# Kernel tuning notes

Measured on AMD Instinct MI355X. Metric: run time of the kernel, lower is better.

Reference implementation:

```python
import jax, jax.numpy as jnp
import numpy as np

B, C, H, W = 8, 3, 64, 64
HORIZON = 32
WIDTH = 32
M1 = M2 = M3 = 8
N_LAYERS = 4
C_OUT = 3


def setup_inputs() -> dict:
    key = jax.random.key(0)
    ks = jax.random.split(key, 16)
    scale = 1.0 / (WIDTH * WIDTH)
    wshape = (N_LAYERS, 4, WIDTH, WIDTH, M1, M2, M3)
    return {
        "x_t": jax.random.normal(ks[0], (B, C, H, W), dtype=jnp.float32),
        "p_w": jax.random.normal(ks[1], (WIDTH, C + 3), dtype=jnp.float32) * 0.1,
        "p_b": jnp.zeros((WIDTH,), dtype=jnp.float32),
        "spec_wr": scale * jax.random.normal(ks[2], wshape, dtype=jnp.float32),
        "spec_wi": scale * jax.random.normal(ks[3], wshape, dtype=jnp.float32),
        "pw_w": jax.random.normal(ks[4], (N_LAYERS, WIDTH, WIDTH), dtype=jnp.float32) * 0.1,
        "pw_b": jnp.zeros((N_LAYERS, WIDTH), dtype=jnp.float32),
        "q1_w": jax.random.normal(ks[5], (2 * WIDTH, WIDTH), dtype=jnp.float32) * 0.1,
        "q1_b": jnp.zeros((2 * WIDTH,), dtype=jnp.float32),
        "q2_w": jax.random.normal(ks[6], (C_OUT, 2 * WIDTH), dtype=jnp.float32) * 0.1,
        "q2_b": jnp.zeros((C_OUT,), dtype=jnp.float32),
        "horizon": HORIZON,
    }


def _conv1x1(x, w, b):
    # x: [b, i, x, y, z], w: [o, i] -> [b, o, x, y, z]
    return jnp.einsum("oi,bixyz->boxyz", w, x) + b[None, :, None, None, None]


def _spectral_conv3d(x, wr, wi):
    # x: [b, i, H, W, T]; wr/wi: [4, i, o, m1, m2, m3]
    h, w_, t = x.shape[-3], x.shape[-2], x.shape[-1]
    xf = jnp.fft.rfftn(x, axes=(-3, -2, -1))  # [b, i, H, W, T//2+1]
    wc = (wr + 1j * wi).astype(xf.dtype)
    m1 = min(M1, xf.shape[-3]); m2 = min(M2, xf.shape[-2]); m3 = min(M3, xf.shape[-1])
    mul = lambda a, ww: jnp.einsum("bixyz,ioxyz->boxyz", a, ww)
    out = jnp.zeros((x.shape[0], wr.shape[2]) + xf.shape[2:], dtype=xf.dtype)
    out = out.at[:, :, :m1, :m2, :m3].set(mul(xf[:, :, :m1, :m2, :m3], wc[0, :, :, :m1, :m2, :m3]))
    out = out.at[:, :, -m1:, :m2, :m3].set(mul(xf[:, :, -m1:, :m2, :m3], wc[1, :, :, :m1, :m2, :m3]))
    out = out.at[:, :, :m1, -m2:, :m3].set(mul(xf[:, :, :m1, -m2:, :m3], wc[2, :, :, :m1, :m2, :m3]))
    out = out.at[:, :, -m1:, -m2:, :m3].set(mul(xf[:, :, -m1:, -m2:, :m3], wc[3, :, :, :m1, :m2, :m3]))
    return jnp.fft.irfftn(out, s=(h, w_, t), axes=(-3, -2, -1))


def _grid_3d(b, h, w, t, dtype):
    gy = jnp.broadcast_to(jnp.linspace(0.0, 1.0, h, dtype=dtype)[None, None, :, None, None], (b, 1, h, w, t))
    gx = jnp.broadcast_to(jnp.linspace(0.0, 1.0, w, dtype=dtype)[None, None, None, :, None], (b, 1, h, w, t))
    gt = jnp.broadcast_to(jnp.linspace(0.0, 1.0, t, dtype=dtype)[None, None, None, None, :], (b, 1, h, w, t))
    return jnp.concatenate([gy, gx, gt], axis=1)


def reference(x_t, p_w, p_b, spec_wr, spec_wi, pw_w, pw_b, q1_w, q1_b, q2_w, q2_b, horizon):
    b, c, h, w = x_t.shape
    x = jnp.broadcast_to(x_t[..., None], (b, c, h, w, horizon))  # repeat over time
    grid = _grid_3d(b, h, w, horizon, x_t.dtype)
    x = jnp.concatenate([x, grid], axis=1)  # [b, c+3, h, w, t]
    x = _conv1x1(x, p_w, p_b)
    for l in range(N_LAYERS):
        x = jax.nn.gelu(
            _spectral_conv3d(x, spec_wr[l], spec_wi[l]) + _conv1x1(x, pw_w[l], pw_b[l]),
            approximate=False,
        )
    x = _conv1x1(x, q1_w, q1_b)
    x = jax.nn.gelu(x, approximate=False)
    x = _conv1x1(x, q2_w, q2_b)
    # [b, c_out, h, w, t] -> [b, t, c_out, h, w]
    return jnp.transpose(x, (0, 4, 1, 2, 3))
```

## Files before the change

kernel.cpp:

```cpp
#include <hip/hip_runtime.h>
#include <math.h>


#define TWO_PI 6.2831853071795864769f

typedef short bf16x8 __attribute__((ext_vector_type(8)));
typedef float f32x4 __attribute__((ext_vector_type(4)));
typedef float v2f __attribute__((ext_vector_type(2)));

__device__ __forceinline__ f32x4 mfma16(bf16x8 a, bf16x8 b, f32x4 c) {
    return __builtin_amdgcn_mfma_f32_16x16x32_bf16(a, b, c, 0, 0, 0);
}

__device__ __forceinline__ void split8(float4 a, float4 b, bf16x8& h, bf16x8& l) {
    float f[8] = {a.x, a.y, a.z, a.w, b.x, b.y, b.z, b.w};
    #pragma unroll
    for (int i = 0; i < 8; ++i) {
        unsigned u = __float_as_uint(f[i]);
        h[i] = (short)(u >> 16);
        float hf = __uint_as_float(u & 0xFFFF0000u);
        float lf = f[i] - hf;
        l[i] = (short)(__float_as_uint(lf) >> 16);
    }
}

__device__ __forceinline__ v2f make2(float x) { v2f r; r.x = x; r.y = x; return r; }
__device__ __forceinline__ v2f fma2(v2f a, v2f b, v2f c) { return __builtin_elementwise_fma(a, b, c); }

__device__ __forceinline__ v2f gelu2(v2f v) {
    v2f u = v * 0.70710678118654752f;
    v2f a = __builtin_elementwise_abs(u);
    v2f den = fma2(a, make2(0.3275911f), make2(1.0f));
    v2f t; t.x = __builtin_amdgcn_rcpf(den.x); t.y = __builtin_amdgcn_rcpf(den.y);
    v2f p = t * (0.254829592f + t * (-0.284496736f + t * (1.421413741f +
            t * (-1.453152027f + t * 1.061405429f))));
    v2f e; e.x = __expf(-u.x * u.x); e.y = __expf(-u.y * u.y);
    v2f m = fma2(-p, e, make2(1.0f));
    v2f erfu = __builtin_elementwise_copysign(m, u);
    return 0.5f * v * (1.0f + erfu);
}

__device__ __forceinline__ void gelu4(f32x4& q) {
    v2f p0; p0.x = q[0]; p0.y = q[1];
    v2f p1; p1.x = q[2]; p1.y = q[3];
    p0 = gelu2(p0); p1 = gelu2(p1);
    q[0] = p0.x; q[1] = p0.y; q[2] = p1.x; q[3] = p1.y;
}

#define GOERTZEL_CONSTS \
    const float C2[8] = {2.0f, 1.9615705608f, 1.8477590650f, 1.6629392246f, \
                         1.4142135624f, 1.1111404660f, 0.7653668647f, 0.3901806440f}; \
    const float CK[8] = {1.0f, 0.9807852804f, 0.9238795325f, 0.8314696123f, \
                         0.7071067812f, 0.5555702330f, 0.3826834324f, 0.1950903220f}; \
    const float SK[8] = {0.0f, 0.1950903220f, 0.3826834324f, 0.5555702330f, \
                         0.7071067812f, 0.8314696123f, 0.9238795325f, 0.9807852804f};

#define GOERTZEL_EO(col, STRIDE, emit_ptr) { \
    GOERTZEL_CONSTS \
    float s1[8], s2[8]; \
    _Pragma("unroll") \
    for (int k = 0; k < 8; ++k) { s1[k] = 0.f; s2[k] = 0.f; } \
    for (int tt = 0; tt < 16; ++tt) { \
        float x0 = (col)[tt * (STRIDE)], x1 = (col)[(tt + 16) * (STRIDE)]; \
        float ev = x0 + x1, ov = x0 - x1; \
        _Pragma("unroll") \
        for (int k = 0; k < 8; ++k) { \
            float v = (k & 1) ? ov : ev; \
            float s0 = v + C2[k] * s1[k] - s2[k]; \
            s2[k] = s1[k]; s1[k] = s0; \
        } \
    } \
    _Pragma("unroll") \
    for (int k = 0; k < 8; ++k) { \
        float R = CK[k] * s1[k] - s2[k]; \
        float I = SK[k] * s1[k]; \
        if (k & 1) { R = -R; I = -I; } \
        (emit_ptr)[k] = make_float2(R, I); \
    } }

__global__ __launch_bounds__(256) void k_lift(const float* __restrict__ xt,
                                              const float* __restrict__ pw,
                                              const float* __restrict__ pb,
                                              float* __restrict__ X,
                                              float2* __restrict__ T1) {
    __shared__ float xs[8448];
    int g = blockIdx.x;
    int spt = g & 511, b = g >> 9;
    int sp0 = spt * 8;
    int y = sp0 >> 6, x0 = sp0 & 63;
    int tid = threadIdx.x;
    int t = tid & 31, spl = tid >> 5;
    int sp = sp0 + spl;
    float a0 = xt[(b * 3 + 0) * 4096 + sp];
    float a1 = xt[(b * 3 + 1) * 4096 + sp];
    float a2 = xt[(b * 3 + 2) * 4096 + sp];
    float gy = y * (1.0f / 63.0f), gx = (x0 + spl) * (1.0f / 63.0f), gt = t * (1.0f / 31.0f);
    float v[32];
    #pragma unroll
    for (int c = 0; c < 32; ++c) {
        const float* w = pw + c * 6;
        v[c] = pb[c] + w[0] * a0 + w[1] * a1 + w[2] * a2
             + w[3] * gy + w[4] * gx + w[5] * gt;
    }
    float* xg = X + (((long)(b * 4096 + sp)) * 32 + t) * 32;
    #pragma unroll
    for (int j = 0; j < 8; ++j)
        ((float4*)xg)[j] = make_float4(v[4*j], v[4*j+1], v[4*j+2], v[4*j+3]);
    float* row = xs + (spl * 32 + t) * 33;
    #pragma unroll
    for (int c = 0; c < 32; ++c) row[c] = v[c];
    __syncthreads();
    int c = tid & 31, sl = tid >> 5;
    const float* col = xs + (sl * 32) * 33 + c;
    float2* ob = T1 + ((long)(b * 32 + c) * 4096 + sp0 + sl) * 8;
    GOERTZEL_EO(col, 33, ob)
}

__global__ __launch_bounds__(256) void k_xdft(const float2* __restrict__ T1, float2* __restrict__ T2) {
    __shared__ float2 s[1024];
    __shared__ float2 tw[64];
    int g = blockIdx.x;
    int ypair = g & 31; int bc = g >> 5;
    long base = ((long)bc * 64 + ypair * 2) * 512;
    int tid = threadIdx.x;
    for (int k = tid; k < 1024; k += 256) s[k] = T1[base + k];
    if (tid < 64) { float sn, cs; __sincosf(tid * (TWO_PI / 64.0f), &sn, &cs); tw[tid] = make_float2(cs, sn); }
    __syncthreads();
    #pragma unroll
    for (int r = 0; r < 2; ++r) {
        int j = tid + r * 256;
        int half = j >> 8, rem = j & 255;
        int idx = half * 512 + rem;
        float2 a = s[idx], b2 = s[idx + 256];
        s[idx] = make_float2(a.x + b2.x, a.y + b2.y);
        s[idx + 256] = make_float2(a.x - b2.x, a.y - b2.y);
    }
    __syncthreads();
    int half = tid >> 7, jj = tid & 127;
    int kxi = jj >> 3, kt = jj & 7;
    int kx = kxi < 8 ? kxi : kxi + 48;
    const float2* row = s + half * 512 + (kx & 1) * 256;
    float sr = 0.f, si = 0.f;
    for (int x = 0; x < 32; ++x) {
        float2 w = tw[(kx * x) & 63];
        float2 a = row[x * 8 + kt];
        sr += a.x * w.x + a.y * w.y;
        si += a.y * w.x - a.x * w.y;
    }
    T2[((long)bc * 64 + ypair * 2 + half) * 128 + jj] = make_float2(sr, si);
}

__global__ __launch_bounds__(128) void k_ydft(const float2* __restrict__ T2, float2* __restrict__ T3) {
    __shared__ float2 s[512];
    __shared__ float2 tw[64];
    int g = blockIdx.x;
    int kx = g & 15; int bc = g >> 4;
    int tid = threadIdx.x;
    for (int k = tid; k < 512; k += 128) {
        int y = k >> 3, kt = k & 7;
        s[k] = T2[((long)bc * 64 + y) * 128 + kx * 8 + kt];
    }
    if (tid < 64) { float sn, cs; __sincosf(tid * (TWO_PI / 64.0f), &sn, &cs); tw[tid] = make_float2(cs, sn); }
    __syncthreads();
    #pragma unroll
    for (int r = 0; r < 2; ++r) {
        int j = tid + r * 128;
        float2 a = s[j], b2 = s[j + 256];
        s[j] = make_float2(a.x + b2.x, a.y + b2.y);
        s[j + 256] = make_float2(a.x - b2.x, a.y - b2.y);
    }
    __syncthreads();
    int kyi = tid >> 3, kt = tid & 7;
    int ky = kyi < 8 ? kyi : kyi + 48;
    const float2* row = s + (ky & 1) * 256;
    float sr = 0.f, si = 0.f;
    for (int y = 0; y < 32; ++y) {
        float2 w = tw[(ky * y) & 63];
        float2 a = row[y * 8 + kt];
        sr += a.x * w.x + a.y * w.y;
        si += a.y * w.x - a.x * w.y;
    }
    T3[((long)bc * 256 + kyi * 16 + kx) * 8 + kt] = make_float2(sr, si);
}

__global__ __launch_bounds__(256) void k_mix2(const float2* __restrict__ T3,
                                              const float* __restrict__ wr,
                                              const float* __restrict__ wi,
                                              float2* __restrict__ T4, int layer) {
    __shared__ float2 s[2304];
    int mode = blockIdx.x;
    int kyi = mode >> 4, kxi = mode & 15;
    int tid = threadIdx.x;
    {
        int bb = tid >> 5, i = tid & 31;
        const float2* src = T3 + ((long)(bb * 32 + i) * 256 + mode) * 8;
        float2* dst = s + (i * 8 + bb) * 9;
        #pragma unroll
        for (int k = 0; k < 8; ++k) dst[k] = src[k];
    }
    __syncthreads();
    int corner = (kyi >= 8 ? 1 : 0) + (kxi >= 8 ? 2 : 0);
    long wbase = (long)(layer * 4 + corner) * 524288 + (long)(kyi & 7) * 64 + (long)(kxi & 7) * 8;
    int o = tid >> 3, kt = tid & 7;
    long wb = wbase + (long)o * 512 + kt;
    float2 acc[8];
    #pragma unroll
    for (int bb = 0; bb < 8; ++bb) acc[bb] = make_float2(0.f, 0.f);
    for (int i = 0; i < 32; ++i) {
        float r = wr[wb + (long)i * 16384], im = wi[wb + (long)i * 16384];
        #pragma unroll
        for (int bb = 0; bb < 8; ++bb) {
            float2 a = s[(i * 8 + bb) * 9 + kt];
            acc[bb].x += a.x * r - a.y * im;
            acc[bb].y += a.x * im + a.y * r;
        }
    }
    #pragma unroll
    for (int bb = 0; bb < 8; ++bb)
        T4[((long)(bb * 32 + o) * 256 + mode) * 8 + kt] = acc[bb];
}

__global__ __launch_bounds__(256) void k_invy(const float2* __restrict__ T4, float2* __restrict__ T5) {
    __shared__ float2 s[128];
    __shared__ float2 tw[64];
    __shared__ float2 pmP[56], pmM[56];
    int g = blockIdx.x;
    int kx = g & 15; int bc = g >> 4;
    int tid = threadIdx.x;
    if (tid < 128) {
        int kyi = tid >> 3, kt = tid & 7;
        s[tid] = T4[((long)bc * 256 + kyi * 16 + kx) * 8 + kt];
    } else if (tid < 192) {
        int m = tid - 128; float sn, cs; __sincosf(m * (TWO_PI / 64.0f), &sn, &cs); tw[m] = make_float2(cs, sn);
    }
    __syncthreads();
    if (tid < 56) {
        int j = (tid >> 3) + 1, kt = tid & 7;
        float2 a = s[j * 8 + kt], b2 = s[(16 - j) * 8 + kt];
        pmP[tid] = make_float2(a.x + b2.x, a.y + b2.y);
        pmM[tid] = make_float2(a.x - b2.x, a.y - b2.y);
    }
    __syncthreads();
    #pragma unroll
    for (int r = 0; r < 2; ++r) {
        int j = tid + r * 256;
        int y = j >> 3, kt = j & 7;
        float2 A0 = s[kt], A8 = s[64 + kt];
        float2 w8 = tw[(8 * y) & 63];
        float sr = A0.x + A8.x * w8.x + A8.y * w8.y;
        float si = A0.y + A8.y * w8.x - A8.x * w8.y;
        #pragma unroll
        for (int jj = 1; jj < 8; ++jj) {
            float2 w = tw[(jj * y) & 63];
            float2 P = pmP[(jj - 1) * 8 + kt], M = pmM[(jj - 1) * 8 + kt];
            sr += P.x * w.x - M.y * w.y;
            si += P.y * w.x + M.x * w.y;
        }
        T5[((long)bc * 64 + y) * 128 + kx * 8 + kt] = make_float2(sr, si);
    }
}

__global__ __launch_bounds__(256) void k_invx(const float2* __restrict__ T5, float2* __restrict__ T6) {
    __shared__ float2 s[128];
    __shared__ float2 tw[64];
    __shared__ float2 pmP[56], pmM[56];
    int g = blockIdx.x;
    int tid = threadIdx.x;
    if (tid < 128) {
        s[tid] = T5[(long)g * 128 + tid];
    } else if (tid < 192) {
        int m = tid - 128; float sn, cs; __sincosf(m * (TWO_PI / 64.0f), &sn, &cs); tw[m] = make_float2(cs, sn);
    }
    __syncthreads();
    if (tid < 56) {
        int j = (tid >> 3) + 1, kt = tid & 7;
        float2 a = s[j * 8 + kt], b2 = s[(16 - j) * 8 + kt];
        pmP[tid] = make_float2(a.x + b2.x, a.y + b2.y);
        pmM[tid] = make_float2(a.x - b2.x, a.y - b2.y);
    }
    __syncthreads();
    #pragma unroll
    for (int r = 0; r < 2; ++r) {
        int j = tid + r * 256;
        int x = j >> 3, kt = j & 7;
        float2 A0 = s[kt], A8 = s[64 + kt];
        float2 w8 = tw[(8 * x) & 63];
        float sr = A0.x + A8.x * w8.x + A8.y * w8.y;
        float si = A0.y + A8.y * w8.x - A8.x * w8.y;
        #pragma unroll
        for (int jj = 1; jj < 8; ++jj) {
            float2 w = tw[(jj * x) & 63];
            float2 P = pmP[(jj - 1) * 8 + kt], M = pmM[(jj - 1) * 8 + kt];
            sr += P.x * w.x - M.y * w.y;
            si += P.y * w.x + M.x * w.y;
        }
        T6[(long)g * 512 + j] = make_float2(sr, si);
    }
}

__device__ __forceinline__ void make_invt_A(int l15, int quad, bf16x8 Ah[2], bf16x8 Al[2]) {
    #pragma unroll
    for (int th = 0; th < 2; ++th) {
        float m[8];
        if (quad < 2) {
            int tt = th * 16 + l15;
            #pragma unroll
            for (int kk = 0; kk < 4; ++kk) {
                int k = quad * 4 + kk;
                float sn, cs;
                __sincosf((float)(k * tt) * (TWO_PI / 32.0f), &sn, &cs);
                float w = k ? 2.0f : 1.0f;
                m[2 * kk] = w * cs;
                m[2 * kk + 1] = -w * sn;
            }
        } else {
            #pragma unroll
            for (int j = 0; j < 8; ++j) m[j] = 0.f;
        }
        split8(make_float4(m[0], m[1], m[2], m[3]),
               make_float4(m[4], m[5], m[6], m[7]), Ah[th], Al[th]);
    }
}

__global__ __launch_bounds__(256) void k_fuse3(float* __restrict__ X, const float2* __restrict__ T6,
                                               const float* __restrict__ pww,
                                               const float* __restrict__ pwb,
                                               float2* __restrict__ T1, int layer) {
    __shared__ float smem[9216];
    float2* ts = (float2*)smem;
    int g = blockIdx.x;
    int spt = g & 511, b = g >> 9;
    int sp0 = spt * 8;
    int tid = threadIdx.x;
    {
        int o = tid >> 3, spl = tid & 7;
        const float4* src = (const float4*)(T6 + ((long)(b * 32 + o) * 4096 + sp0 + spl) * 8);
        float4* dst = (float4*)(ts + o * 66 + spl * 8);
        const float S = 1.0f / 131072.0f;
        #pragma unroll
        for (int j = 0; j < 4; ++j) {
            float4 q = src[j];
            dst[j] = make_float4(q.x * S, q.y * S, q.z * S, q.w * S);
        }
    }
    int wave = tid >> 6, lane = tid & 63, l15 = lane & 15, quad = lane >> 4;
    int wb = wave * 64;
    const float* wl = pww + layer * 1024;
    const float* bl = pwb + layer * 32;
    bf16x8 wah[2], wal[2];
    f32x4 acc[2][4];
    #pragma unroll
    for (int mt = 0; mt < 2; ++mt) {
        const float4* p = (const float4*)(wl + (mt * 16 + l15) * 32 + quad * 8);
        split8(p[0], p[1], wah[mt], wal[mt]);
        float4 bv = *(const float4*)(bl + mt * 16 + quad * 4);
        f32x4 bi; bi[0] = bv.x; bi[1] = bv.y; bi[2] = bv.z; bi[3] = bv.w;
        #pragma unroll
        for (int nt = 0; nt < 4; ++nt) acc[mt][nt] = bi;
    }
    #pragma unroll
    for (int nt = 0; nt < 4; ++nt) {
        int pt = wb + nt * 16 + l15;
        int spl = pt >> 5, t = pt & 31;
        const float4* xp = (const float4*)(X + (((long)(b * 4096 + sp0 + spl)) * 32 + t) * 32 + quad * 8);
        bf16x8 bh, blo; split8(xp[0], xp[1], bh, blo);
        #pragma unroll
        for (int mt = 0; mt < 2; ++mt) {
            acc[mt][nt] = mfma16(wah[mt], bh, acc[mt][nt]);
            acc[mt][nt] = mfma16(wal[mt], bh, acc[mt][nt]);
            acc[mt][nt] = mfma16(wah[mt], blo, acc[mt][nt]);
        }
    }
    bf16x8 Ah[2], Al[2];
    make_invt_A(l15, quad, Ah, Al);
    __syncthreads();
    bf16x8 Bh[2][2], Bl[2][2];
    #pragma unroll
    for (int sph = 0; sph < 2; ++sph) {
        int spl = 2 * wave + sph;
        #pragma unroll
        for (int ch = 0; ch < 2; ++ch) {
            float4 q0 = make_float4(0.f, 0.f, 0.f, 0.f), q1 = q0;
            if (quad < 2) {
                const float4* p = (const float4*)(ts + (ch * 16 + l15) * 66 + spl * 8 + quad * 4);
                q0 = p[0]; q1 = p[1];
            }
            split8(q0, q1, Bh[sph][ch], Bl[sph][ch]);
        }
    }
    __syncthreads();
    #pragma unroll
    for (int sph = 0; sph < 2; ++sph) {
        int spl = 2 * wave + sph;
        #pragma unroll
        for (int ch = 0; ch < 2; ++ch)
            #pragma unroll
            for (int th = 0; th < 2; ++th) {
                f32x4 d = {0.f, 0.f, 0.f, 0.f};
                d = mfma16(Ah[th], Bh[sph][ch], d);
                d = mfma16(Al[th], Bh[sph][ch], d);
                d = mfma16(Ah[th], Bl[sph][ch], d);
                float* wp = smem + (spl * 32 + th * 16 + quad * 4) * 36 + ch * 16 + l15;
                wp[0] = d[0]; wp[36] = d[1]; wp[72] = d[2]; wp[108] = d[3];
            }
    }
    __syncthreads();
    #pragma unroll
    for (int mt = 0; mt < 2; ++mt)
        #pragma unroll
        for (int nt = 0; nt < 4; ++nt) {
            int pt = wb + nt * 16 + l15;
            int spl = pt >> 5, t = pt & 31;
            float4 sp4 = *(const float4*)(smem + (spl * 32 + t) * 36 + mt * 16 + quad * 4);
            acc[mt][nt][0] += sp4.x; acc[mt][nt][1] += sp4.y;
            acc[mt][nt][2] += sp4.z; acc[mt][nt][3] += sp4.w;
        }
    #pragma unroll
    for (int mt = 0; mt < 2; ++mt)
        #pragma unroll
        for (int nt = 0; nt < 4; ++nt) gelu4(acc[mt][nt]);
    #pragma unroll
    for (int mt = 0; mt < 2; ++mt)
        #pragma unroll
        for (int nt = 0; nt < 4; ++nt) {
            int pt = wb + nt * 16 + l15;
            int spl = pt >> 5, t = pt & 31;
            int o0 = mt * 16 + quad * 4;
            float4 w4 = make_float4(acc[mt][nt][0], acc[mt][nt][1], acc[mt][nt][2], acc[mt][nt][3]);
            *(float4*)(X + (((long)(b * 4096 + sp0 + spl)) * 32 + t) * 32 + o0) = w4;
            *(float4*)(smem + (spl * 32 + t) * 36 + o0) = w4;
        }
    __syncthreads();
    int c = tid & 31, sl = tid >> 5;
    const float* col = smem + (sl * 32) * 36 + c;
    float2* ob = T1 + ((long)(b * 32 + c) * 4096 + sp0 + sl) * 8;
    GOERTZEL_EO(col, 36, ob)
}

__global__ __launch_bounds__(256) void k_fuse3_last(const float* __restrict__ X, const float2* __restrict__ T6,
                                                    const float* __restrict__ pww, const float* __restrict__ pwb,
                                                    const float* __restrict__ q1w, const float* __restrict__ q1b,
                                                    const float* __restrict__ q2w, const float* __restrict__ q2b,
                                                    float* __restrict__ out) {
    __shared__ float smem[9408];
    float2* ts = (float2*)smem;
    int g = blockIdx.x;
    int spt = g & 511, b = g >> 9;
    int sp0 = spt * 8;
    int tid = threadIdx.x;
    {
        int o = tid >> 3, spl = tid & 7;
        const float4* src = (const float4*)(T6 + ((long)(b * 32 + o) * 4096 + sp0 + spl) * 8);
        float4* dst = (float4*)(ts + o * 66 + spl * 8);
        const float S = 1.0f / 131072.0f;
        #pragma unroll
        for (int j = 0; j < 4; ++j) {
            float4 q = src[j];
            dst[j] = make_float4(q.x * S, q.y * S, q.z * S, q.w * S);
        }
    }
    if (tid < 192) smem[9216 + tid] = q2w[tid];
    int wave = tid >> 6, lane = tid & 63, l15 = lane & 15, quad = lane >> 4;
    int wb = wave * 64;
    const float* wl = pww + 3 * 1024;
    const float* bl = pwb + 3 * 32;
    bf16x8 wah[2], wal[2];
    f32x4 acc[2][4];
    #pragma unroll
    for (int mt = 0; mt < 2; ++mt) {
        const float4* p = (const float4*)(wl + (mt * 16 + l15) * 32 + quad * 8);
        split8(p[0], p[1], wah[mt], wal[mt]);
        float4 bv = *(const float4*)(bl + mt * 16 + quad * 4);
        f32x4 bi; bi[0] = bv.x; bi[1] = bv.y; bi[2] = bv.z; bi[3] = bv.w;
        #pragma unroll
        for (int nt = 0; nt < 4; ++nt) acc[mt][nt] = bi;
    }
    #pragma unroll
    for (int nt = 0; nt < 4; ++nt) {
        int pt = wb + nt * 16 + l15;
        int spl = pt >> 5, t = pt & 31;
        const float4* xp = (const float4*)(X + (((long)(b * 4096 + sp0 + spl)) * 32 + t) * 32 + quad * 8);
        bf16x8 bh, blo; split8(xp[0], xp[1], bh, blo);
        #pragma unroll
        for (int mt = 0; mt < 2; ++mt) {
            acc[mt][nt] = mfma16(wah[mt], bh, acc[mt][nt]);
            acc[mt][nt] = mfma16(wal[mt], bh, acc[mt][nt]);
            acc[mt][nt] = mfma16(wah[mt], blo, acc[mt][nt]);
        }
    }
    bf16x8 Ah[2], Al[2];
    make_invt_A(l15, quad, Ah, Al);
    __syncthreads();
    bf16x8 Bh[2][2], Bl[2][2];
    #pragma unroll
    for (int sph = 0; sph < 2; ++sph) {
        int spl = 2 * wave + sph;
        #pragma unroll
        for (int ch = 0; ch < 2; ++ch) {
            float4 q0 = make_float4(0.f, 0.f, 0.f, 0.f), q1 = q0;
            if (quad < 2) {
                const float4* p = (const float4*)(ts + (ch * 16 + l15) * 66 + spl * 8 + quad * 4);
                q0 = p[0]; q1 = p[1];
            }
            split8(q0, q1, Bh[sph][ch], Bl[sph][ch]);
        }
    }
    __syncthreads();
    #pragma unroll
    for (int sph = 0; sph < 2; ++sph) {
        int spl = 2 * wave + sph;
        #pragma unroll
        for (int ch = 0; ch < 2; ++ch)
            #pragma unroll
            for (int th = 0; th < 2; ++th) {
                f32x4 d = {0.f, 0.f, 0.f, 0.f};
                d = mfma16(Ah[th], Bh[sph][ch], d);
                d = mfma16(Al[th], Bh[sph][ch], d);
                d = mfma16(Ah[th], Bl[sph][ch], d);
                float* wp = smem + (spl * 32 + th * 16 + quad * 4) * 36 + ch * 16 + l15;
                wp[0] = d[0]; wp[36] = d[1]; wp[72] = d[2]; wp[108] = d[3];
            }
    }
    __syncthreads();
    #pragma unroll
    for (int mt = 0; mt < 2; ++mt)
        #pragma unroll
        for (int nt = 0; nt < 4; ++nt) {
            int pt = wb + nt * 16 + l15;
            int spl = pt >> 5, t = pt & 31;
            float4 sp4 = *(const float4*)(smem + (spl * 32 + t) * 36 + mt * 16 + quad * 4);
            acc[mt][nt][0] += sp4.x; acc[mt][nt][1] += sp4.y;
            acc[mt][nt][2] += sp4.z; acc[mt][nt][3] += sp4.w;
        }
    #pragma unroll
    for (int mt = 0; mt < 2; ++mt)
        #pragma unroll
        for (int nt = 0; nt < 4; ++nt) gelu4(acc[mt][nt]);
    #pragma unroll
    for (int mt = 0; mt < 2; ++mt)
        #pragma unroll
        for (int nt = 0; nt < 4; ++nt) {
            int pt = wb + nt * 16 + l15;
            int o0 = mt * 16 + quad * 4;
            *(float4*)(smem + pt * 36 + o0) =
                make_float4(acc[mt][nt][0], acc[mt][nt][1], acc[mt][nt][2], acc[mt][nt][3]);
        }
    __syncthreads();
    bf16x8 qah[4], qal[4];
    f32x4 qbv[4];
    #pragma unroll
    for (int mt = 0; mt < 4; ++mt) {
        const float4* p = (const float4*)(q1w + (mt * 16 + l15) * 32 + quad * 8);
        split8(p[0], p[1], qah[mt], qal[mt]);
        float4 bv = *(const float4*)(q1b + mt * 16 + quad * 4);
        qbv[mt][0] = bv.x; qbv[mt][1] = bv.y; qbv[mt][2] = bv.z; qbv[mt][3] = bv.w;
    }
    const float* q2l = smem + 9216;
    float q2b0 = q2b[0], q2b1 = q2b[1], q2b2 = q2b[2];
    float oc0[4], oc1[4], oc2[4];
    #pragma unroll
    for (int nt = 0; nt < 4; ++nt) {
        int pt = wb + nt * 16 + l15;
        const float4* bp = (const float4*)(smem + pt * 36 + quad * 8);
        bf16x8 bh, blo; split8(bp[0], bp[1], bh, blo);
        float p0 = 0.f, p1 = 0.f, p2 = 0.f;
        #pragma unroll
        for (int mt = 0; mt < 4; ++mt) {
            f32x4 h = qbv[mt];
            h = mfma16(qah[mt], bh, h);
            h = mfma16(qal[mt], bh, h);
            h = mfma16(qah[mt], blo, h);
            gelu4(h);
            #pragma unroll
            for (int reg = 0; reg < 4; ++reg) {
                int hh = mt * 16 + quad * 4 + reg;
                p0 += q2l[hh] * h[reg];
                p1 += q2l[64 + hh] * h[reg];
                p2 += q2l[128 + hh] * h[reg];
            }
        }
        p0 += __shfl_xor(p0, 16); p0 += __shfl_xor(p0, 32);
        p1 += __shfl_xor(p1, 16); p1 += __shfl_xor(p1, 32);
        p2 += __shfl_xor(p2, 16); p2 += __shfl_xor(p2, 32);
        oc0[nt] = p0 + q2b0; oc1[nt] = p1 + q2b1; oc2[nt] = p2 + q2b2;
    }
    __syncthreads();
    if (quad == 0) {
        #pragma unroll
        for (int nt = 0; nt < 4; ++nt) {
            int pt = wb + nt * 16 + l15;
            int spl = pt >> 5, t = pt & 31;
            smem[(t * 3 + 0) * 9 + spl] = oc0[nt];
            smem[(t * 3 + 1) * 9 + spl] = oc1[nt];
            smem[(t * 3 + 2) * 9 + spl] = oc2[nt];
        }
    }
    __syncthreads();
    for (int m = tid; m < 768; m += 256) {
        int u = m >> 3, spl = m & 7;
        out[((long)(b * 96 + u)) * 4096 + sp0 + spl] = smem[u * 9 + spl];
    }
}

extern "C" void kernel_launch(void* const* d_in, const int* in_sizes, int n_in,
                              void* d_out, int out_size, void* d_ws, size_t ws_size,
                              hipStream_t stream) {
    const float* xt  = (const float*)d_in[0];
    const float* pw  = (const float*)d_in[1];
    const float* pb  = (const float*)d_in[2];
    const float* swr = (const float*)d_in[3];
    const float* swi = (const float*)d_in[4];
    const float* pww = (const float*)d_in[5];
    const float* pwb = (const float*)d_in[6];
    const float* q1w = (const float*)d_in[7];
    const float* q1b = (const float*)d_in[8];
    const float* q2w = (const float*)d_in[9];
    const float* q2b = (const float*)d_in[10];
    float* out = (float*)d_out;

    float*  X  = (float*)d_ws;
    float2* T1 = (float2*)(X + 33554432);
    float2* T2 = (float2*)((float*)T1 + 16777216);
    float2* T3 = (float2*)((float*)T2 + 4194304);
    float2* T4 = (float2*)((float*)T3 + 1048576);

    k_lift<<<4096, 256, 0, stream>>>(xt, pw, pb, X, T1);
    for (int l = 0; l < 4; ++l) {
        k_xdft<<<8192, 256, 0, stream>>>(T1, T2);
        k_ydft<<<4096, 128, 0, stream>>>(T2, T3);
        k_mix2<<<256, 256, 0, stream>>>(T3, swr, swi, T4, l);
        k_invy<<<4096, 256, 0, stream>>>(T4, T2);
        k_invx<<<16384, 256, 0, stream>>>(T2, T1);
        if (l < 3)
            k_fuse3<<<4096, 256, 0, stream>>>(X, T1, pww, pwb, T1, l);
        else
            k_fuse3_last<<<4096, 256, 0, stream>>>(X, T1, pww, pwb, q1w, q1b, q2w, q2b, out);
    }
}
```

Baseline: 811.5 us.

## Replace Goertzel time-axis DFT with split-bf16 MFMA matrix multiply

The scalar Goertzel recurrence that computed the first 8 time-frequency modes in the lift and fused layer kernels is replaced by a DFT-as-matmul on MFMA units. Activations are packed into hi/lo bf16 pairs in shared memory, and a twiddle matrix is generated per lane and used in three bf16 MFMAs to recover near-fp32 accuracy. This removes the long serial FMA chain per thread, at the cost of extra packing work, an extra barrier, and a small precision change from the 3-term bf16 split.

```diff
diff --git a/kernel.cpp b/kernel.cpp
--- a/kernel.cpp
+++ b/kernel.cpp
@@ -21,6 +21,22 @@
         float hf = __uint_as_float(u & 0xFFFF0000u);
         float lf = f[i] - hf;
         l[i] = (short)(__float_as_uint(lf) >> 16);
+    }
+}
+
+__device__ __forceinline__ unsigned packhl(float f) {
+    unsigned u = __float_as_uint(f);
+    unsigned hi = u & 0xFFFF0000u;
+    float lf = f - __uint_as_float(hi);
+    return hi | (__float_as_uint(lf) >> 16);
+}
+
+__device__ __forceinline__ void unpack8(uint4 a, uint4 b, bf16x8& h, bf16x8& l) {
+    unsigned u[8] = {a.x, a.y, a.z, a.w, b.x, b.y, b.z, b.w};
+    #pragma unroll
+    for (int i = 0; i < 8; ++i) {
+        h[i] = (short)(u[i] >> 16);
+        l[i] = (short)(u[i] & 0xFFFFu);
     }
 }
 
@@ -47,43 +63,49 @@
     q[0] = p0.x; q[1] = p0.y; q[2] = p1.x; q[3] = p1.y;
 }
 
-#define GOERTZEL_CONSTS \
-    const float C2[8] = {2.0f, 1.9615705608f, 1.8477590650f, 1.6629392246f, \
-                         1.4142135624f, 1.1111404660f, 0.7653668647f, 0.3901806440f}; \
-    const float CK[8] = {1.0f, 0.9807852804f, 0.9238795325f, 0.8314696123f, \
-                         0.7071067812f, 0.5555702330f, 0.3826834324f, 0.1950903220f}; \
-    const float SK[8] = {0.0f, 0.1950903220f, 0.3826834324f, 0.5555702330f, \
-                         0.7071067812f, 0.8314696123f, 0.9238795325f, 0.9807852804f};
-
-#define GOERTZEL_EO(col, STRIDE, emit_ptr) { \
-    GOERTZEL_CONSTS \
-    float s1[8], s2[8]; \
-    _Pragma("unroll") \
-    for (int k = 0; k < 8; ++k) { s1[k] = 0.f; s2[k] = 0.f; } \
-    for (int tt = 0; tt < 16; ++tt) { \
-        float x0 = (col)[tt * (STRIDE)], x1 = (col)[(tt + 16) * (STRIDE)]; \
-        float ev = x0 + x1, ov = x0 - x1; \
-        _Pragma("unroll") \
-        for (int k = 0; k < 8; ++k) { \
-            float v = (k & 1) ? ov : ev; \
-            float s0 = v + C2[k] * s1[k] - s2[k]; \
-            s2[k] = s1[k]; s1[k] = s0; \
-        } \
-    } \
-    _Pragma("unroll") \
-    for (int k = 0; k < 8; ++k) { \
-        float R = CK[k] * s1[k] - s2[k]; \
-        float I = SK[k] * s1[k]; \
-        if (k & 1) { R = -R; I = -I; } \
-        (emit_ptr)[k] = make_float2(R, I); \
-    } }
+__device__ __forceinline__ void make_fwd_A(int l15, int quad, bf16x8& Gh, bf16x8& Gl) {
+    int k = l15 >> 1;
+    float s0, c0, ds, dc;
+    __sincosf((float)(k * quad * 8) * (TWO_PI / 32.0f), &s0, &c0);
+    __sincosf((float)k * (TWO_PI / 32.0f), &ds, &dc);
+    float m[8];
+    float cc = c0, ss = s0;
+    #pragma unroll
+    for (int j = 0; j < 8; ++j) {
+        m[j] = (l15 & 1) ? -ss : cc;
+        float nc = cc * dc - ss * ds;
+        float ns = ss * dc + cc * ds;
+        cc = nc; ss = ns;
+    }
+    split8(make_float4(m[0], m[1], m[2], m[3]),
+           make_float4(m[4], m[5], m[6], m[7]), Gh, Gl);
+}
+
+__device__ __forceinline__ void fwd_tdft(const unsigned* up, int b, int sp0,
+                                         float2* __restrict__ T1,
+                                         int wb, int l15, int quad,
+                                         bf16x8 Gh, bf16x8 Gl) {
+    #pragma unroll
+    for (int nt = 0; nt < 4; ++nt) {
+        int r = wb + nt * 16 + l15;
+        const uint4* p = (const uint4*)(up + r * 36 + quad * 8);
+        bf16x8 bh, bl; unpack8(p[0], p[1], bh, bl);
+        f32x4 d = {0.f, 0.f, 0.f, 0.f};
+        d = mfma16(Gh, bh, d);
+        d = mfma16(Gl, bh, d);
+        d = mfma16(Gh, bl, d);
+        int c = r & 31, spl = r >> 5;
+        float4* ob = (float4*)(T1 + ((long)(b * 32 + c) * 4096 + sp0 + spl) * 8 + quad * 2);
+        *ob = make_float4(d[0], d[1], d[2], d[3]);
+    }
+}
 
 __global__ __launch_bounds__(256) void k_lift(const float* __restrict__ xt,
                                               const float* __restrict__ pw,
                                               const float* __restrict__ pb,
                                               float* __restrict__ X,
                                               float2* __restrict__ T1) {
-    __shared__ float xs[8448];
+    __shared__ unsigned xs[9216];
     int g = blockIdx.x;
     int spt = g & 511, b = g >> 9;
     int sp0 = spt * 8;
@@ -106,14 +128,13 @@
     #pragma unroll
     for (int j = 0; j < 8; ++j)
         ((float4*)xg)[j] = make_float4(v[4*j], v[4*j+1], v[4*j+2], v[4*j+3]);
-    float* row = xs + (spl * 32 + t) * 33;
-    #pragma unroll
-    for (int c = 0; c < 32; ++c) row[c] = v[c];
-    __syncthreads();
-    int c = tid & 31, sl = tid >> 5;
-    const float* col = xs + (sl * 32) * 33 + c;
-    float2* ob = T1 + ((long)(b * 32 + c) * 4096 + sp0 + sl) * 8;
-    GOERTZEL_EO(col, 33, ob)
+    #pragma unroll
+    for (int c = 0; c < 32; ++c)
+        xs[(spl * 32 + c) * 36 + t] = packhl(v[c]);
+    int wave = tid >> 6, lane = tid & 63, l15 = lane & 15, quad = lane >> 4;
+    bf16x8 Gh, Gl; make_fwd_A(l15, quad, Gh, Gl);
+    __syncthreads();
+    fwd_tdft(xs, b, sp0, T1, wave * 64, l15, quad, Gh, Gl);
 }
 
 __global__ __launch_bounds__(256) void k_xdft(const float2* __restrict__ T1, float2* __restrict__ T2) {
@@ -415,10 +436,13 @@
             acc[mt][nt][0] += sp4.x; acc[mt][nt][1] += sp4.y;
             acc[mt][nt][2] += sp4.z; acc[mt][nt][3] += sp4.w;
         }
+    __syncthreads();
+    bf16x8 Gh, Gl; make_fwd_A(l15, quad, Gh, Gl);
     #pragma unroll
     for (int mt = 0; mt < 2; ++mt)
         #pragma unroll
         for (int nt = 0; nt < 4; ++nt) gelu4(acc[mt][nt]);
+    unsigned* up = (unsigned*)smem;
     #pragma unroll
     for (int mt = 0; mt < 2; ++mt)
         #pragma unroll
@@ -428,13 +452,13 @@
             int o0 = mt * 16 + quad * 4;
             float4 w4 = make_float4(acc[mt][nt][0], acc[mt][nt][1], acc[mt][nt][2], acc[mt][nt][3]);
             *(float4*)(X + (((long)(b * 4096 + sp0 + spl)) * 32 + t) * 32 + o0) = w4;
-            *(float4*)(smem + (spl * 32 + t) * 36 + o0) = w4;
-        }
-    __syncthreads();
-    int c = tid & 31, sl = tid >> 5;
-    const float* col = smem + (sl * 32) * 36 + c;
-    float2* ob = T1 + ((long)(b * 32 + c) * 4096 + sp0 + sl) * 8;
-    GOERTZEL_EO(col, 36, ob)
+            up[(spl * 32 + o0 + 0) * 36 + t] = packhl(w4.x);
+            up[(spl * 32 + o0 + 1) * 36 + t] = packhl(w4.y);
+            up[(spl * 32 + o0 + 2) * 36 + t] = packhl(w4.z);
+            up[(spl * 32 + o0 + 3) * 36 + t] = packhl(w4.w);
+        }
+    __syncthreads();
+    fwd_tdft(up, b, sp0, T1, wb, l15, quad, Gh, Gl);
 }
 
 __global__ __launch_bounds__(256) void k_fuse3_last(const float* __restrict__ X, const float2* __restrict__ T6,
```

After: 787.1 us. 1.03x faster.
